# Optimization experiments

Hardware: AMD Instinct MI355X
Metric: run time of the kernel (lower is better)

Reference implementation:

```python
import jax, jax.numpy as jnp
import numpy as np

T, B, I, H = 2048, 64, 512, 512
SIGMA = 0.01


def setup_inputs() -> dict:
    key = jax.random.key(0)
    ks = jax.random.split(key, 9)
    d = {
        "X": jax.random.normal(ks[0], (T, B, I), dtype=jnp.float32),
        "W_xf": jax.random.normal(ks[1], (I, H), dtype=jnp.float32) * SIGMA,
        "W_hf": jax.random.normal(ks[2], (H, H), dtype=jnp.float32) * SIGMA,
        "b_f": jnp.ones((H,), dtype=jnp.float32),
        "W_xi": jax.random.normal(ks[3], (I, H), dtype=jnp.float32) * SIGMA,
        "W_hi": jax.random.normal(ks[4], (H, H), dtype=jnp.float32) * SIGMA,
        "b_i": jnp.zeros((H,), dtype=jnp.float32),
        "W_xo": jax.random.normal(ks[5], (I, H), dtype=jnp.float32) * SIGMA,
        "W_ho": jax.random.normal(ks[6], (H, H), dtype=jnp.float32) * SIGMA,
        "b_o": jnp.zeros((H,), dtype=jnp.float32),
        "W_xc": jax.random.normal(ks[7], (I, H), dtype=jnp.float32) * SIGMA,
        "W_hc": jax.random.normal(ks[8], (H, H), dtype=jnp.float32) * SIGMA,
        "b_c": jnp.zeros((H,), dtype=jnp.float32),
    }
    return d


def reference(X, W_xf, W_hf, b_f, W_xi, W_hi, b_i, W_xo, W_ho, b_o, W_xc, W_hc, b_c):
    batch = X.shape[1]
    hidden = W_hf.shape[0]
    # Fuse the 4 input-side GEMMs into one [T*B, I] @ [I, 4H] GEMM (same math,
    # just batched over time since X is not part of the recurrence).
    W_x = jnp.concatenate([W_xf, W_xi, W_xo, W_xc], axis=1)           # [I, 4H]
    W_h = jnp.concatenate([W_hf, W_hi, W_ho, W_hc], axis=1)           # [H, 4H]
    b = jnp.concatenate([b_f, b_i, b_o, b_c], axis=0)                 # [4H]
    Xg = jnp.einsum('tbi,ih->tbh', X, W_x) + b                        # [T, B, 4H]

    h0 = jnp.zeros((batch, hidden), dtype=X.dtype)
    c0 = jnp.zeros((batch, hidden), dtype=X.dtype)

    def step(carry, xg):
        h, c = carry
        g = xg + h @ W_h                                              # [B, 4H]
        f = jax.nn.sigmoid(g[:, 0 * hidden:1 * hidden])
        i = jax.nn.sigmoid(g[:, 1 * hidden:2 * hidden])
        o = jax.nn.sigmoid(g[:, 2 * hidden:3 * hidden])
        c_hat = jnp.tanh(g[:, 3 * hidden:4 * hidden])
        c_new = f * c + i * c_hat
        h_new = o * jnp.tanh(c_new)
        return (h_new, c_new), h_new

    (h_T, c_T), outputs = jax.lax.scan(step, (h0, c0), Xg)
    return outputs, h_T, c_T
```

## Files before the change

kernel.cpp:

```cpp
#include <hip/hip_runtime.h>
#include <stdint.h>


typedef __attribute__((ext_vector_type(8))) short short8;
typedef __attribute__((ext_vector_type(4))) float f32x4;

#define T_STEPS 2048
#define GB 4
#define GH 64
#define FSTRIDE 16

__device__ __forceinline__ unsigned short f2bf(float f) {
  unsigned int x = __float_as_uint(f);
  x += 0x7fffu + ((x >> 16) & 1u);
  return (unsigned short)(x >> 16);
}
__device__ __forceinline__ float bf2f(unsigned short u) {
  return __uint_as_float(((unsigned int)u) << 16);
}
__device__ __forceinline__ void gl2lds16(const void* g, void* lds) {
  __builtin_amdgcn_global_load_lds(
      (const __attribute__((address_space(1))) void*)(uintptr_t)g,
      (__attribute__((address_space(3))) void*)(unsigned int)(uintptr_t)lds,
      16, 0, 0);
}


__global__ __launch_bounds__(256) void cast_x_kernel(
    const float* __restrict__ X, unsigned short* __restrict__ Xb) {
  long long i = ((long long)blockIdx.x * 256 + threadIdx.x) * 8;
  float4 a = *(const float4*)(X + i);
  float4 b = *(const float4*)(X + i + 4);
  union { short8 v; unsigned short u[8]; } o;
  o.u[0] = f2bf(a.x); o.u[1] = f2bf(a.y); o.u[2] = f2bf(a.z); o.u[3] = f2bf(a.w);
  o.u[4] = f2bf(b.x); o.u[5] = f2bf(b.y); o.u[6] = f2bf(b.z); o.u[7] = f2bf(b.w);
  *(short8*)(Xb + i) = o.v;
}

__global__ __launch_bounds__(256) void pack_w_kernel(
    const float* __restrict__ Wf, const float* __restrict__ Wi,
    const float* __restrict__ Wo, const float* __restrict__ Wc,
    unsigned short* __restrict__ Wt) {
  int n = blockIdx.x;
  int g = n >> 9, h = n & 511;
  const float* W = (g == 0) ? Wf : (g == 1) ? Wi : (g == 2) ? Wo : Wc;
  for (int k = threadIdx.x; k < 512; k += 256)
    Wt[(size_t)n * 512 + k] = f2bf(W[(size_t)k * 512 + h]);
}

__global__ __launch_bounds__(256) void init_kernel(unsigned short* hbuf, int* flags) {
  int i = blockIdx.x * 256 + threadIdx.x;
  if (i < 2 * 64 * 512) hbuf[i] = 0;
  if (i < GB * GH * FSTRIDE) flags[i] = 0;
}

__global__ __launch_bounds__(256) void gemm_xg_kernel(
    const unsigned short* __restrict__ A, const unsigned short* __restrict__ Bt,
    unsigned short* __restrict__ C) {
  __shared__ unsigned short As[128 * 64];
  __shared__ unsigned short Bs[128 * 64];
  const int tid = threadIdx.x;
  const int lane = tid & 63, wave = tid >> 6;
  const int bm = blockIdx.x, bn = blockIdx.y;
  const int wm = (wave & 1) * 64, wn = (wave >> 1) * 64;

  f32x4 acc[4][4];
#pragma unroll
  for (int i = 0; i < 4; ++i)
#pragma unroll
    for (int j = 0; j < 4; ++j) acc[i][j] = (f32x4){0.f, 0.f, 0.f, 0.f};

  for (int kt = 0; kt < 512; kt += 64) {
    __syncthreads();
#pragma unroll
    for (int r = 0; r < 4; ++r) {
      int chunk = r * 256 + tid;
      int row = chunk >> 3, c8 = chunk & 7;
      gl2lds16(A + ((size_t)(bm * 128 + row) * 512 + kt + c8 * 8),
               (void*)(As + (size_t)(r * 256 + wave * 64) * 8));
      gl2lds16(Bt + ((size_t)(bn * 128 + row) * 512 + kt + c8 * 8),
               (void*)(Bs + (size_t)(r * 256 + wave * 64) * 8));
    }
    __syncthreads();
#pragma unroll
    for (int kc = 0; kc < 64; kc += 32) {
      const int ko = kc + (lane >> 4) * 8;
      short8 av[4], bv[4];
#pragma unroll
      for (int mt = 0; mt < 4; ++mt)
        av[mt] = *(const short8*)(As + (wm + mt * 16 + (lane & 15)) * 64 + ko);
#pragma unroll
      for (int nt = 0; nt < 4; ++nt)
        bv[nt] = *(const short8*)(Bs + (wn + nt * 16 + (lane & 15)) * 64 + ko);
#pragma unroll
      for (int mt = 0; mt < 4; ++mt)
#pragma unroll
        for (int nt = 0; nt < 4; ++nt)
          acc[mt][nt] = __builtin_amdgcn_mfma_f32_16x16x32_bf16(
              av[mt], bv[nt], acc[mt][nt], 0, 0, 0);
    }
  }
  const int q = lane >> 4, cidx = lane & 15;
#pragma unroll
  for (int mt = 0; mt < 4; ++mt)
#pragma unroll
    for (int nt = 0; nt < 4; ++nt)
#pragma unroll
      for (int r = 0; r < 4; ++r) {
        int row = wm + mt * 16 + q * 4 + r;
        int col = wn + nt * 16 + cidx;
        C[(size_t)(bm * 128 + row) * 2048 + bn * 128 + col] = f2bf(acc[mt][nt][r]);
      }
}

__global__ __launch_bounds__(256) void lstm_rec_kernel(
    const unsigned short* __restrict__ Xg,
    const unsigned short* __restrict__ Wht,
    const float* __restrict__ b_f, const float* __restrict__ b_i,
    const float* __restrict__ b_o, const float* __restrict__ b_c,
    float* __restrict__ out, unsigned short* hbuf, int* flags) {
  const int tid = threadIdx.x;
  const int lane = tid & 63, wave = tid >> 6;
  const int gb = blockIdx.x >> 6;
  const int gh = blockIdx.x & 63;

  __shared__ unsigned short Wl[32][520];
  __shared__ float Cred[4][16][33];

  for (int idx = tid; idx < 32 * 64; idx += 256) {
    int cc = idx >> 6, k8 = idx & 63;
    int n = (cc >> 3) * 512 + gh * 8 + (cc & 7);
    short8 v = *(const short8*)(Wht + (size_t)n * 512 + k8 * 8);
    *(short8*)(&Wl[cc][k8 * 8]) = v;
  }

  float creg = 0.f;
  float bias0 = 0.f, bias1 = 0.f, bias2 = 0.f, bias3 = 0.f;
  int bb = 0, jj = 0;
  if (tid < 128) {
    bb = tid >> 3; jj = tid & 7;
    int col = gh * 8 + jj;
    bias0 = b_f[col]; bias1 = b_i[col]; bias2 = b_o[col]; bias3 = b_c[col];
  }
  __syncthreads();

  const int myflag = (gb * GH + gh) * FSTRIDE;

  for (int t = 0; t < T_STEPS; ++t) {
    float xg0 = 0.f, xg1 = 0.f, xg2 = 0.f, xg3 = 0.f;
    if (tid < 128) {
      const unsigned short* xr =
          Xg + ((size_t)t * 64 + gb * 16 + bb) * 2048 + gh * 8 + jj;
      xg0 = bf2f(xr[0]); xg1 = bf2f(xr[512]); xg2 = bf2f(xr[1024]); xg3 = bf2f(xr[1536]);
    }
    if (t > 0) {
      if (tid < GH) {
        const int* fp = flags + (gb * GH + tid) * FSTRIDE;
        while (__hip_atomic_load(fp, __ATOMIC_RELAXED, __HIP_MEMORY_SCOPE_AGENT) < t)
          __builtin_amdgcn_s_sleep(1);
      }
      __syncthreads();
      __builtin_amdgcn_fence(__ATOMIC_ACQUIRE, "workgroup");
    }
    const unsigned short* hrow =
        hbuf + ((size_t)(t & 1) * 64 * 512) + (size_t)gb * 16 * 512;
    f32x4 acc0 = {0.f, 0.f, 0.f, 0.f}, acc1 = {0.f, 0.f, 0.f, 0.f};
    const int m = lane & 15, quad = lane >> 4;
#pragma unroll
    for (int kc = 0; kc < 128; kc += 32) {
      int k = wave * 128 + kc + quad * 8;
      const unsigned long long* ap =
          (const unsigned long long*)(hrow + (size_t)m * 512 + k);
      union { short8 v; unsigned long long q[2]; } au;
      au.q[0] = __hip_atomic_load(ap, __ATOMIC_RELAXED, __HIP_MEMORY_SCOPE_AGENT);
      au.q[1] = __hip_atomic_load(ap + 1, __ATOMIC_RELAXED, __HIP_MEMORY_SCOPE_AGENT);
      short8 bfr0 = *(const short8*)(&Wl[m][k]);
      short8 bfr1 = *(const short8*)(&Wl[16 + m][k]);
      acc0 = __builtin_amdgcn_mfma_f32_16x16x32_bf16(au.v, bfr0, acc0, 0, 0, 0);
      acc1 = __builtin_amdgcn_mfma_f32_16x16x32_bf16(au.v, bfr1, acc1, 0, 0, 0);
    }
#pragma unroll
    for (int r = 0; r < 4; ++r) {
      Cred[wave][quad * 4 + r][m] = acc0[r];
      Cred[wave][quad * 4 + r][16 + m] = acc1[r];
    }
    __syncthreads();
    if (tid < 128) {
      float gf = Cred[0][bb][jj] + Cred[1][bb][jj] + Cred[2][bb][jj] + Cred[3][bb][jj];
      float gi = Cred[0][bb][8+jj] + Cred[1][bb][8+jj] + Cred[2][bb][8+jj] + Cred[3][bb][8+jj];
      float go = Cred[0][bb][16+jj] + Cred[1][bb][16+jj] + Cred[2][bb][16+jj] + Cred[3][bb][16+jj];
      float gc = Cred[0][bb][24+jj] + Cred[1][bb][24+jj] + Cred[2][bb][24+jj] + Cred[3][bb][24+jj];
      gf += bias0 + xg0; gi += bias1 + xg1; go += bias2 + xg2; gc += bias3 + xg3;
      float f  = 1.f / (1.f + __expf(-gf));
      float ii = 1.f / (1.f + __expf(-gi));
      float oo = 1.f / (1.f + __expf(-go));
      float ch = 1.f - 2.f / (1.f + __expf(2.f * gc));
      creg = f * creg + ii * ch;
      float tc = 1.f - 2.f / (1.f + __expf(2.f * creg));
      float h = oo * tc;
      size_t orow = ((size_t)t * 64 + gb * 16 + bb) * 512 + gh * 8 + jj;
      out[orow] = h;
      __hip_atomic_store(hbuf + ((size_t)((t + 1) & 1) * 64 * 512) +
                             (size_t)(gb * 16 + bb) * 512 + gh * 8 + jj,
                         f2bf(h), __ATOMIC_RELAXED, __HIP_MEMORY_SCOPE_AGENT);
      if (t == T_STEPS - 1) {
        size_t base = (size_t)T_STEPS * 64 * 512;
        out[base + (size_t)(gb * 16 + bb) * 512 + gh * 8 + jj] = h;
        out[base + 64 * 512 + (size_t)(gb * 16 + bb) * 512 + gh * 8 + jj] = creg;
      }
    }
    __syncthreads();
    __builtin_amdgcn_fence(__ATOMIC_RELEASE, "workgroup");
    if (tid == 0)
      __hip_atomic_store(flags + myflag, t + 1, __ATOMIC_RELAXED,
                         __HIP_MEMORY_SCOPE_AGENT);
  }
}


extern "C" void kernel_launch(void* const* d_in, const int* in_sizes, int n_in,
                              void* d_out, int out_size, void* d_ws, size_t ws_size,
                              hipStream_t stream) {
  const float* X    = (const float*)d_in[0];
  const float* W_xf = (const float*)d_in[1];
  const float* W_hf = (const float*)d_in[2];
  const float* b_f  = (const float*)d_in[3];
  const float* W_xi = (const float*)d_in[4];
  const float* W_hi = (const float*)d_in[5];
  const float* b_i  = (const float*)d_in[6];
  const float* W_xo = (const float*)d_in[7];
  const float* W_ho = (const float*)d_in[8];
  const float* b_o  = (const float*)d_in[9];
  const float* W_xc = (const float*)d_in[10];
  const float* W_hc = (const float*)d_in[11];
  const float* b_c  = (const float*)d_in[12];
  float* out = (float*)d_out;

  char* ws = (char*)d_ws;
  unsigned short* Xb   = (unsigned short*)(ws + 0LL);
  unsigned short* Xg   = (unsigned short*)(ws + 134217728LL);
  unsigned short* Wxt  = (unsigned short*)(ws + 671088640LL);
  unsigned short* Wht  = (unsigned short*)(ws + 673185792LL);
  unsigned short* hbuf = (unsigned short*)(ws + 675282944LL);
  int* flags           = (int*)(ws + 675414016LL);

  cast_x_kernel<<<dim3(32768), dim3(256), 0, stream>>>(X, Xb);
  pack_w_kernel<<<dim3(2048), dim3(256), 0, stream>>>(W_xf, W_xi, W_xo, W_xc, Wxt);
  pack_w_kernel<<<dim3(2048), dim3(256), 0, stream>>>(W_hf, W_hi, W_ho, W_hc, Wht);
  init_kernel<<<dim3(256), dim3(256), 0, stream>>>(hbuf, flags);
  gemm_xg_kernel<<<dim3(1024, 16), dim3(256), 0, stream>>>(Xb, Wxt, Xg);
  lstm_rec_kernel<<<dim3(256), dim3(256), 0, stream>>>(Xg, Wht, b_f, b_i, b_o, b_c,
                                                       out, hbuf, flags);
}
```

Before: 6.006 ms.

## Fuse input GEMM and recurrence into one persistent kernel with progress flags

```diff
diff --git a/kernel.cpp b/kernel.cpp
--- a/kernel.cpp
+++ b/kernel.cpp
@@ -6,8 +6,10 @@
 typedef __attribute__((ext_vector_type(4))) float f32x4;
 
 #define T_STEPS 2048
-#define GB 4
-#define GH 64
+#define GBN 4
+#define GHN 16
+#define NREC 64
+#define NWORK 192
 #define FSTRIDE 16
 
 __device__ __forceinline__ unsigned short f2bf(float f) {
@@ -24,6 +26,11 @@
       (__attribute__((address_space(3))) void*)(unsigned int)(uintptr_t)lds,
       16, 0, 0);
 }
+
+union Smem {
+  struct { unsigned short As[128 * 64]; unsigned short Bs[128 * 64]; } g;
+  struct { unsigned short Wl[128][520]; float Cg[4][16][33]; } r;
+};
 
 
 __global__ __launch_bounds__(256) void cast_x_kernel(
@@ -48,167 +55,201 @@
     Wt[(size_t)n * 512 + k] = f2bf(W[(size_t)k * 512 + h]);
 }
 
-__global__ __launch_bounds__(256) void init_kernel(unsigned short* hbuf, int* flags) {
+__global__ __launch_bounds__(256) void init_kernel(unsigned short* hbuf,
+                                                   int* flags, int* xgprog) {
   int i = blockIdx.x * 256 + threadIdx.x;
   if (i < 2 * 64 * 512) hbuf[i] = 0;
-  if (i < GB * GH * FSTRIDE) flags[i] = 0;
-}
-
-__global__ __launch_bounds__(256) void gemm_xg_kernel(
-    const unsigned short* __restrict__ A, const unsigned short* __restrict__ Bt,
-    unsigned short* __restrict__ C) {
-  __shared__ unsigned short As[128 * 64];
-  __shared__ unsigned short Bs[128 * 64];
+  if (i < NREC * FSTRIDE) flags[i] = 0;
+  if (i < 1024) xgprog[i] = 0;
+}
+
+
+__global__ __launch_bounds__(256, 1) void lstm_fused_kernel(
+    const unsigned short* __restrict__ Xb,
+    const unsigned short* __restrict__ Wxt,
+    const unsigned short* __restrict__ Wht,
+    unsigned short* __restrict__ Xg,
+    const float* __restrict__ b_f, const float* __restrict__ b_i,
+    const float* __restrict__ b_o, const float* __restrict__ b_c,
+    float* __restrict__ out, unsigned short* hbuf, int* flags, int* xgprog) {
+  __shared__ Smem sm;
   const int tid = threadIdx.x;
   const int lane = tid & 63, wave = tid >> 6;
-  const int bm = blockIdx.x, bn = blockIdx.y;
-  const int wm = (wave & 1) * 64, wn = (wave >> 1) * 64;
-
-  f32x4 acc[4][4];
-#pragma unroll
-  for (int i = 0; i < 4; ++i)
-#pragma unroll
-    for (int j = 0; j < 4; ++j) acc[i][j] = (f32x4){0.f, 0.f, 0.f, 0.f};
-
-  for (int kt = 0; kt < 512; kt += 64) {
+  const int wg = blockIdx.x;
+
+  if (wg >= NREC) {
+    const int q = wg - NREC;
+    const int wm = (wave & 1) * 64, wn = (wave >> 1) * 64;
+    for (int tau = q; tau < 16384; tau += NWORK) {
+      const int mt = tau >> 4, nt = tau & 15;
+      f32x4 acc[4][4];
+#pragma unroll
+      for (int i = 0; i < 4; ++i)
+#pragma unroll
+        for (int j = 0; j < 4; ++j) acc[i][j] = (f32x4){0.f, 0.f, 0.f, 0.f};
+
+      for (int kt = 0; kt < 512; kt += 64) {
+        __syncthreads();
+#pragma unroll
+        for (int r = 0; r < 4; ++r) {
+          int chunk = r * 256 + tid;
+          int row = chunk >> 3, c8 = chunk & 7;
+          gl2lds16(Xb + ((size_t)(mt * 128 + row) * 512 + kt + c8 * 8),
+                   (void*)(sm.g.As + (size_t)(r * 256 + wave * 64) * 8));
+          gl2lds16(Wxt + ((size_t)(nt * 128 + row) * 512 + kt + c8 * 8),
+                   (void*)(sm.g.Bs + (size_t)(r * 256 + wave * 64) * 8));
+        }
+        __syncthreads();
+#pragma unroll
+        for (int kc = 0; kc < 64; kc += 32) {
+          const int ko = kc + (lane >> 4) * 8;
+          short8 av[4], bv[4];
+#pragma unroll
+          for (int mi = 0; mi < 4; ++mi)
+            av[mi] = *(const short8*)(sm.g.As + (wm + mi * 16 + (lane & 15)) * 64 + ko);
+#pragma unroll
+          for (int ni = 0; ni < 4; ++ni)
+            bv[ni] = *(const short8*)(sm.g.Bs + (wn + ni * 16 + (lane & 15)) * 64 + ko);
+#pragma unroll
+          for (int mi = 0; mi < 4; ++mi)
+#pragma unroll
+            for (int ni = 0; ni < 4; ++ni)
+              acc[mi][ni] = __builtin_amdgcn_mfma_f32_16x16x32_bf16(
+                  av[mi], bv[ni], acc[mi][ni], 0, 0, 0);
+        }
+      }
+      const int q4 = lane >> 4, cidx = lane & 15;
+#pragma unroll
+      for (int mi = 0; mi < 4; ++mi)
+#pragma unroll
+        for (int ni = 0; ni < 4; ++ni)
+#pragma unroll
+          for (int r = 0; r < 4; ++r) {
+            int row = wm + mi * 16 + q4 * 4 + r;
+            int col = wn + ni * 16 + cidx;
+            __hip_atomic_store(
+                Xg + (size_t)(mt * 128 + row) * 2048 + nt * 128 + col,
+                f2bf(acc[mi][ni][r]), __ATOMIC_RELAXED, __HIP_MEMORY_SCOPE_AGENT);
+          }
+      __syncthreads();
+      if (tid == 0)
+        __hip_atomic_fetch_add(xgprog + mt, 1, __ATOMIC_RELAXED,
+                               __HIP_MEMORY_SCOPE_AGENT);
+    }
+    return;
+  }
+
+  const int gb = wg >> 4;
+  const int gh = wg & 15;
+  const unsigned* Xgu = (const unsigned*)Xg;
+
+  for (int idx = tid; idx < 128 * 64; idx += 256) {
+    int cc = idx >> 6, k8 = idx & 63;
+    int n = (cc >> 5) * 512 + gh * 32 + (cc & 31);
+    short8 v = *(const short8*)(Wht + (size_t)n * 512 + k8 * 8);
+    *(short8*)(&sm.r.Wl[cc][k8 * 8]) = v;
+  }
+
+  const int bb = tid >> 4, rem = tid & 15, jj2 = rem * 2;
+  const float2 bfv = *(const float2*)(b_f + gh * 32 + jj2);
+  const float2 biv = *(const float2*)(b_i + gh * 32 + jj2);
+  const float2 bov = *(const float2*)(b_o + gh * 32 + jj2);
+  const float2 bcv = *(const float2*)(b_c + gh * 32 + jj2);
+  float c0 = 0.f, c1 = 0.f;
+
+  const int m = lane & 15, quad = lane >> 4;
+  const unsigned short* wl0 = &sm.r.Wl[wave * 32 + m][0];
+  const unsigned short* wl1 = &sm.r.Wl[wave * 32 + 16 + m][0];
+  const int myflag = wg * FSTRIDE;
+  __syncthreads();
+
+  for (int t = 0; t < T_STEPS; ++t) {
+    if (wave == 0) {
+      for (;;) {
+        int ok = 1;
+        if (lane < GHN) {
+          int v = __hip_atomic_load(flags + (gb * GHN + lane) * FSTRIDE,
+                                    __ATOMIC_RELAXED, __HIP_MEMORY_SCOPE_AGENT);
+          ok = (v >= t);
+        } else if (lane == GHN) {
+          int p = __hip_atomic_load(xgprog + (t >> 1), __ATOMIC_RELAXED,
+                                    __HIP_MEMORY_SCOPE_AGENT);
+          ok = (p >= 16);
+        }
+        if (__all(ok)) break;
+        __builtin_amdgcn_s_sleep(1);
+      }
+    }
     __syncthreads();
-#pragma unroll
-    for (int r = 0; r < 4; ++r) {
-      int chunk = r * 256 + tid;
-      int row = chunk >> 3, c8 = chunk & 7;
-      gl2lds16(A + ((size_t)(bm * 128 + row) * 512 + kt + c8 * 8),
-               (void*)(As + (size_t)(r * 256 + wave * 64) * 8));
-      gl2lds16(Bt + ((size_t)(bn * 128 + row) * 512 + kt + c8 * 8),
-               (void*)(Bs + (size_t)(r * 256 + wave * 64) * 8));
-    }
-    __syncthreads();
-#pragma unroll
-    for (int kc = 0; kc < 64; kc += 32) {
-      const int ko = kc + (lane >> 4) * 8;
-      short8 av[4], bv[4];
-#pragma unroll
-      for (int mt = 0; mt < 4; ++mt)
-        av[mt] = *(const short8*)(As + (wm + mt * 16 + (lane & 15)) * 64 + ko);
-#pragma unroll
-      for (int nt = 0; nt < 4; ++nt)
-        bv[nt] = *(const short8*)(Bs + (wn + nt * 16 + (lane & 15)) * 64 + ko);
-#pragma unroll
-      for (int mt = 0; mt < 4; ++mt)
-#pragma unroll
-        for (int nt = 0; nt < 4; ++nt)
-          acc[mt][nt] = __builtin_amdgcn_mfma_f32_16x16x32_bf16(
-              av[mt], bv[nt], acc[mt][nt], 0, 0, 0);
-    }
-  }
-  const int q = lane >> 4, cidx = lane & 15;
-#pragma unroll
-  for (int mt = 0; mt < 4; ++mt)
-#pragma unroll
-    for (int nt = 0; nt < 4; ++nt)
-#pragma unroll
-      for (int r = 0; r < 4; ++r) {
-        int row = wm + mt * 16 + q * 4 + r;
-        int col = wn + nt * 16 + cidx;
-        C[(size_t)(bm * 128 + row) * 2048 + bn * 128 + col] = f2bf(acc[mt][nt][r]);
-      }
-}
-
-__global__ __launch_bounds__(256) void lstm_rec_kernel(
-    const unsigned short* __restrict__ Xg,
-    const unsigned short* __restrict__ Wht,
-    const float* __restrict__ b_f, const float* __restrict__ b_i,
-    const float* __restrict__ b_o, const float* __restrict__ b_c,
-    float* __restrict__ out, unsigned short* hbuf, int* flags) {
-  const int tid = threadIdx.x;
-  const int lane = tid & 63, wave = tid >> 6;
-  const int gb = blockIdx.x >> 6;
-  const int gh = blockIdx.x & 63;
-
-  __shared__ unsigned short Wl[32][520];
-  __shared__ float Cred[4][16][33];
-
-  for (int idx = tid; idx < 32 * 64; idx += 256) {
-    int cc = idx >> 6, k8 = idx & 63;
-    int n = (cc >> 3) * 512 + gh * 8 + (cc & 7);
-    short8 v = *(const short8*)(Wht + (size_t)n * 512 + k8 * 8);
-    *(short8*)(&Wl[cc][k8 * 8]) = v;
-  }
-
-  float creg = 0.f;
-  float bias0 = 0.f, bias1 = 0.f, bias2 = 0.f, bias3 = 0.f;
-  int bb = 0, jj = 0;
-  if (tid < 128) {
-    bb = tid >> 3; jj = tid & 7;
-    int col = gh * 8 + jj;
-    bias0 = b_f[col]; bias1 = b_i[col]; bias2 = b_o[col]; bias3 = b_c[col];
-  }
-  __syncthreads();
-
-  const int myflag = (gb * GH + gh) * FSTRIDE;
-
-  for (int t = 0; t < T_STEPS; ++t) {
-    float xg0 = 0.f, xg1 = 0.f, xg2 = 0.f, xg3 = 0.f;
-    if (tid < 128) {
-      const unsigned short* xr =
-          Xg + ((size_t)t * 64 + gb * 16 + bb) * 2048 + gh * 8 + jj;
-      xg0 = bf2f(xr[0]); xg1 = bf2f(xr[512]); xg2 = bf2f(xr[1024]); xg3 = bf2f(xr[1536]);
-    }
-    if (t > 0) {
-      if (tid < GH) {
-        const int* fp = flags + (gb * GH + tid) * FSTRIDE;
-        while (__hip_atomic_load(fp, __ATOMIC_RELAXED, __HIP_MEMORY_SCOPE_AGENT) < t)
-          __builtin_amdgcn_s_sleep(1);
-      }
-      __syncthreads();
-      __builtin_amdgcn_fence(__ATOMIC_ACQUIRE, "workgroup");
-    }
+    __builtin_amdgcn_fence(__ATOMIC_ACQUIRE, "workgroup");
+
+    unsigned xgw[4];
+    {
+      size_t xrow = ((size_t)t * 64 + gb * 16 + bb) * 1024 + gh * 16 + rem;
+#pragma unroll
+      for (int g = 0; g < 4; ++g)
+        xgw[g] = __hip_atomic_load(Xgu + xrow + g * 256, __ATOMIC_RELAXED,
+                                   __HIP_MEMORY_SCOPE_AGENT);
+    }
+
     const unsigned short* hrow =
         hbuf + ((size_t)(t & 1) * 64 * 512) + (size_t)gb * 16 * 512;
     f32x4 acc0 = {0.f, 0.f, 0.f, 0.f}, acc1 = {0.f, 0.f, 0.f, 0.f};
-    const int m = lane & 15, quad = lane >> 4;
-#pragma unroll
-    for (int kc = 0; kc < 128; kc += 32) {
-      int k = wave * 128 + kc + quad * 8;
+#pragma unroll
+    for (int kk = 0; kk < 512; kk += 32) {
+      int k = kk + quad * 8;
       const unsigned long long* ap =
           (const unsigned long long*)(hrow + (size_t)m * 512 + k);
-      union { short8 v; unsigned long long q[2]; } au;
-      au.q[0] = __hip_atomic_load(ap, __ATOMIC_RELAXED, __HIP_MEMORY_SCOPE_AGENT);
-      au.q[1] = __hip_atomic_load(ap + 1, __ATOMIC_RELAXED, __HIP_MEMORY_SCOPE_AGENT);
-      short8 bfr0 = *(const short8*)(&Wl[m][k]);
-      short8 bfr1 = *(const short8*)(&Wl[16 + m][k]);
-      acc0 = __builtin_amdgcn_mfma_f32_16x16x32_bf16(au.v, bfr0, acc0, 0, 0, 0);
-      acc1 = __builtin_amdgcn_mfma_f32_16x16x32_bf16(au.v, bfr1, acc1, 0, 0, 0);
+      union { short8 v; unsigned long long qq[2]; } au;
+      au.qq[0] = __hip_atomic_load(ap, __ATOMIC_RELAXED, __HIP_MEMORY_SCOPE_AGENT);
+      au.qq[1] = __hip_atomic_load(ap + 1, __ATOMIC_RELAXED, __HIP_MEMORY_SCOPE_AGENT);
+      short8 bv0 = *(const short8*)(wl0 + k);
+      short8 bv1 = *(const short8*)(wl1 + k);
+      acc0 = __builtin_amdgcn_mfma_f32_16x16x32_bf16(au.v, bv0, acc0, 0, 0, 0);
+      acc1 = __builtin_amdgcn_mfma_f32_16x16x32_bf16(au.v, bv1, acc1, 0, 0, 0);
     }
 #pragma unroll
     for (int r = 0; r < 4; ++r) {
-      Cred[wave][quad * 4 + r][m] = acc0[r];
-      Cred[wave][quad * 4 + r][16 + m] = acc1[r];
+      sm.r.Cg[wave][quad * 4 + r][m] = acc0[r];
+      sm.r.Cg[wave][quad * 4 + r][16 + m] = acc1[r];
     }
     __syncthreads();
-    if (tid < 128) {
-      float gf = Cred[0][bb][jj] + Cred[1][bb][jj] + Cred[2][bb][jj] + Cred[3][bb][jj];
-      float gi = Cred[0][bb][8+jj] + Cred[1][bb][8+jj] + Cred[2][bb][8+jj] + Cred[3][bb][8+jj];
-      float go = Cred[0][bb][16+jj] + Cred[1][bb][16+jj] + Cred[2][bb][16+jj] + Cred[3][bb][16+jj];
-      float gc = Cred[0][bb][24+jj] + Cred[1][bb][24+jj] + Cred[2][bb][24+jj] + Cred[3][bb][24+jj];
-      gf += bias0 + xg0; gi += bias1 + xg1; go += bias2 + xg2; gc += bias3 + xg3;
-      float f  = 1.f / (1.f + __expf(-gf));
-      float ii = 1.f / (1.f + __expf(-gi));
-      float oo = 1.f / (1.f + __expf(-go));
-      float ch = 1.f - 2.f / (1.f + __expf(2.f * gc));
-      creg = f * creg + ii * ch;
-      float tc = 1.f - 2.f / (1.f + __expf(2.f * creg));
-      float h = oo * tc;
-      size_t orow = ((size_t)t * 64 + gb * 16 + bb) * 512 + gh * 8 + jj;
-      out[orow] = h;
-      __hip_atomic_store(hbuf + ((size_t)((t + 1) & 1) * 64 * 512) +
-                             (size_t)(gb * 16 + bb) * 512 + gh * 8 + jj,
-                         f2bf(h), __ATOMIC_RELAXED, __HIP_MEMORY_SCOPE_AGENT);
-      if (t == T_STEPS - 1) {
-        size_t base = (size_t)T_STEPS * 64 * 512;
-        out[base + (size_t)(gb * 16 + bb) * 512 + gh * 8 + jj] = h;
-        out[base + 64 * 512 + (size_t)(gb * 16 + bb) * 512 + gh * 8 + jj] = creg;
-      }
-    }
+
+    float gf0 = sm.r.Cg[0][bb][jj2]     + bfv.x + bf2f(xgw[0] & 0xffff);
+    float gf1 = sm.r.Cg[0][bb][jj2 + 1] + bfv.y + bf2f(xgw[0] >> 16);
+    float gi0 = sm.r.Cg[1][bb][jj2]     + biv.x + bf2f(xgw[1] & 0xffff);
+    float gi1 = sm.r.Cg[1][bb][jj2 + 1] + biv.y + bf2f(xgw[1] >> 16);
+    float go0 = sm.r.Cg[2][bb][jj2]     + bov.x + bf2f(xgw[2] & 0xffff);
+    float go1 = sm.r.Cg[2][bb][jj2 + 1] + bov.y + bf2f(xgw[2] >> 16);
+    float gc0 = sm.r.Cg[3][bb][jj2]     + bcv.x + bf2f(xgw[3] & 0xffff);
+    float gc1 = sm.r.Cg[3][bb][jj2 + 1] + bcv.y + bf2f(xgw[3] >> 16);
+
+    float f0 = 1.f / (1.f + __expf(-gf0)), f1 = 1.f / (1.f + __expf(-gf1));
+    float i0 = 1.f / (1.f + __expf(-gi0)), i1 = 1.f / (1.f + __expf(-gi1));
+    float o0 = 1.f / (1.f + __expf(-go0)), o1 = 1.f / (1.f + __expf(-go1));
+    float ch0 = 1.f - 2.f / (1.f + __expf(2.f * gc0));
+    float ch1 = 1.f - 2.f / (1.f + __expf(2.f * gc1));
+    c0 = f0 * c0 + i0 * ch0;
+    c1 = f1 * c1 + i1 * ch1;
+    float h0 = o0 * (1.f - 2.f / (1.f + __expf(2.f * c0)));
+    float h1 = o1 * (1.f - 2.f / (1.f + __expf(2.f * c1)));
+
+    float* orow = out + ((size_t)t * 64 + gb * 16 + bb) * 512 + gh * 32 + jj2;
+    *(float2*)orow = make_float2(h0, h1);
+
+    unsigned hp = (unsigned)f2bf(h0) | ((unsigned)f2bf(h1) << 16);
+    __hip_atomic_store(
+        (unsigned*)hbuf + (size_t)((t + 1) & 1) * 16384 +
+            (gb * 16 + bb) * 256 + gh * 16 + rem,
+        hp, __ATOMIC_RELAXED, __HIP_MEMORY_SCOPE_AGENT);
+
+    if (t == T_STEPS - 1) {
+      size_t base = (size_t)T_STEPS * 64 * 512;
+      size_t off = (size_t)(gb * 16 + bb) * 512 + gh * 32 + jj2;
+      *(float2*)(out + base + off) = make_float2(h0, h1);
+      *(float2*)(out + base + 64 * 512 + off) = make_float2(c0, c1);
+    }
+
     __syncthreads();
     __builtin_amdgcn_fence(__ATOMIC_RELEASE, "workgroup");
     if (tid == 0)
@@ -243,12 +284,12 @@
   unsigned short* Wht  = (unsigned short*)(ws + 673185792LL);
   unsigned short* hbuf = (unsigned short*)(ws + 675282944LL);
   int* flags           = (int*)(ws + 675414016LL);
+  int* xgprog          = (int*)(ws + 675418112LL);
 
   cast_x_kernel<<<dim3(32768), dim3(256), 0, stream>>>(X, Xb);
   pack_w_kernel<<<dim3(2048), dim3(256), 0, stream>>>(W_xf, W_xi, W_xo, W_xc, Wxt);
   pack_w_kernel<<<dim3(2048), dim3(256), 0, stream>>>(W_hf, W_hi, W_ho, W_hc, Wht);
-  init_kernel<<<dim3(256), dim3(256), 0, stream>>>(hbuf, flags);
-  gemm_xg_kernel<<<dim3(1024, 16), dim3(256), 0, stream>>>(Xb, Wxt, Xg);
-  lstm_rec_kernel<<<dim3(256), dim3(256), 0, stream>>>(Xg, Wht, b_f, b_i, b_o, b_c,
-                                                       out, hbuf, flags);
-}
+  init_kernel<<<dim3(256), dim3(256), 0, stream>>>(hbuf, flags, xgprog);
+  lstm_fused_kernel<<<dim3(256), dim3(256), 0, stream>>>(
+      Xb, Wxt, Wht, Xg, b_f, b_i, b_o, b_c, out, hbuf, flags, xgprog);
+}
```

Result: slower. 11.38 ms (+89.5%).
